# Kernel tuning notes

Hardware: AMD Instinct MI355X
Metric: run time of the kernel (lower is better)

Reference implementation:

```python
import jax, jax.numpy as jnp
import numpy as np

V, E, H = 50257, 256, 256   # vocab/output_size, embed_size, hidden_size
T, B = 4096, 64             # encoder time steps, batch


def setup_inputs() -> dict:
    key = jax.random.key(0)
    ks = jax.random.split(key, 12)
    s = 0.05
    return {
        "input_ids": jax.random.randint(ks[0], (B,), 0, V),
        "hidden": jax.random.normal(ks[1], (1, B, H), dtype=jnp.float32) * s,
        "encoder_outputs": jax.random.normal(ks[2], (T, B, 2 * H), dtype=jnp.float32) * s,
        # learned parameters (PyTorch Linear convention: W @ x.T, W shape (out, in))
        "emb": jax.random.normal(ks[3], (V, E), dtype=jnp.float32) * s,
        "W_attn": jax.random.normal(ks[4], (H, 3 * H), dtype=jnp.float32) * s,
        "b_attn": jnp.zeros((H,), jnp.float32),
        "v": jax.random.normal(ks[5], (H,), dtype=jnp.float32) * s,
        "W_comb": jax.random.normal(ks[6], (H, 2 * H + E), dtype=jnp.float32) * s,
        "b_comb": jnp.zeros((H,), jnp.float32),
        "W_ih": jax.random.normal(ks[7], (3 * H, H), dtype=jnp.float32) * s,
        "W_hh": jax.random.normal(ks[8], (3 * H, H), dtype=jnp.float32) * s,
        "b_ih": jnp.zeros((3 * H,), jnp.float32),
        "b_hh": jnp.zeros((3 * H,), jnp.float32),
        "W_out": jax.random.normal(ks[9], (V, 3 * H), dtype=jnp.float32) * s,
        "b_out": jnp.zeros((V,), jnp.float32),
    }


def reference(input_ids, hidden, encoder_outputs, emb, W_attn, b_attn, v,
              W_comb, b_comb, W_ih, W_hh, b_ih, b_hh, W_out, b_out):
    Tn, Bn, _ = encoder_outputs.shape
    Hn = hidden.shape[-1]
    embedded = emb[input_ids]                 # (B, E)
    h0 = hidden[0]                            # (B, H)

    # additive (Bahdanau) attention: energies over time axis
    h_rep = jnp.broadcast_to(h0[None], (Tn, Bn, Hn))            # (T, B, H)
    cat = jnp.concatenate([h_rep, encoder_outputs], axis=2)     # (T, B, 3H)
    energies = jnp.tanh(cat @ W_attn.T + b_attn)                # (T, B, H)
    scores = jnp.einsum('tbh,h->tb', energies, v)               # (T, B)
    attn = jax.nn.softmax(scores, axis=0)                       # softmax over time
    context = jnp.einsum('tb,tbd->bd', attn, encoder_outputs)   # (B, 2H)

    # combine context with embedded input
    comb = jnp.concatenate([context, embedded], axis=1) @ W_comb.T + b_comb  # (B, H)

    # single GRU step (PyTorch gate order: r, z, n)
    gx = comb @ W_ih.T + b_ih                 # (B, 3H)
    gh = h0 @ W_hh.T + b_hh                   # (B, 3H)
    xr, xz, xn = jnp.split(gx, 3, axis=1)
    hr, hz, hn = jnp.split(gh, 3, axis=1)
    r = jax.nn.sigmoid(xr + hr)
    z = jax.nn.sigmoid(xz + hz)
    n = jnp.tanh(xn + r * hn)
    h_new = (1.0 - z) * n + z * h0            # (B, H)

    logits = jnp.concatenate([h_new, context], axis=1) @ W_out.T + b_out  # (B, V)
    logp = jax.nn.log_softmax(logits, axis=1)
    return logp, h_new[None]                  # hidden_i shape (1, B, H)
```

## Files before the change

### kernel.cpp

```cpp
#include <hip/hip_runtime.h>
#include <hip/hip_bf16.h>
#include <cstdint>
#include <cstddef>

#define Tn 4096
#define Bn 64
#define Hn 256
#define En 256
#define Vn 50257
#define D2H 512
#define K3H 768

typedef __attribute__((ext_vector_type(8))) short short8;
typedef __attribute__((ext_vector_type(4))) float f32x4;

__device__ __forceinline__ short bfs(float f)
{
    __hip_bfloat16 h = __float2bfloat16(f);
    return *reinterpret_cast<short*>(&h);
}

__device__ __forceinline__ short8 pack8(const float4 x0, const float4 x1)
{
    short8 r;
    r[0] = bfs(x0.x); r[1] = bfs(x0.y); r[2] = bfs(x0.z); r[3] = bfs(x0.w);
    r[4] = bfs(x1.x); r[5] = bfs(x1.y); r[6] = bfs(x1.z); r[7] = bfs(x1.w);
    return r;
}

__device__ __forceinline__ uint2 pack4(const float4 v)
{
    uint2 r;
    r.x = (unsigned)(unsigned short)bfs(v.x) | ((unsigned)(unsigned short)bfs(v.y) << 16);
    r.y = (unsigned)(unsigned short)bfs(v.z) | ((unsigned)(unsigned short)bfs(v.w) << 16);
    return r;
}

__device__ __forceinline__ float bf2f(unsigned short u)
{
    return __uint_as_float(((unsigned)u) << 16);
}


__global__ __launch_bounds__(256) void k1_embed_base(
    const int* __restrict__ ids, const float* __restrict__ hidden,
    const float* __restrict__ emb, const float* __restrict__ W_attn,
    const float* __restrict__ b_attn,
    float* __restrict__ baseB, float* __restrict__ emb_g)
{
    const int b = blockIdx.x, h = threadIdx.x;
    __shared__ float h0[Hn];
    h0[h] = hidden[b * Hn + h];
    __syncthreads();
    float acc = b_attn[h];
    const float* wrow = W_attn + (size_t)h * K3H;
#pragma unroll 8
    for (int k = 0; k < Hn; ++k) acc += wrow[k] * h0[k];
    baseB[b * Hn + h] = acc;
    const int id = ids[b];
    emb_g[b * En + h] = emb[(size_t)id * En + h];
}

__global__ __launch_bounds__(64) void k1b_w2frag(
    const float* __restrict__ W_attn, unsigned short* __restrict__ w2frag)
{
    const int blk = blockIdx.x;
    const int nt = blk >> 4, kb = blk & 15;
    const int l = threadIdx.x, lr = l & 15, lg = l >> 4;
    const int h = nt * 16 + lr;
    const float* src = W_attn + (size_t)h * K3H + Hn + kb * 32 + lg * 8;
    float4 x0 = *reinterpret_cast<const float4*>(src);
    float4 x1 = *reinterpret_cast<const float4*>(src + 4);
    reinterpret_cast<short8*>(w2frag)[(size_t)blk * 64 + l] = pack8(x0, x1);
}

__global__ __launch_bounds__(256, 2) void k2f_attn(
    const float* __restrict__ enc, const unsigned short* __restrict__ w2frag,
    const float* __restrict__ vvec, const float* __restrict__ baseB,
    float* __restrict__ part, float2* __restrict__ meta)
{
    const int tid = threadIdx.x;
    const int bx  = blockIdx.x;
    const int b   = bx & 63;
    const int cid = bx >> 6;
    const int l = tid & 63;
    const int w = tid >> 6;
    const int lr = l & 15, lg = l >> 4;

    __shared__ unsigned short abf[64][520];
    __shared__ float red[64][5];
    __shared__ float wts[64];

    f32x4 acc[4][4];
    const f32x4 zero = {0.f, 0.f, 0.f, 0.f};
#pragma unroll
    for (int mi = 0; mi < 4; ++mi)
#pragma unroll
        for (int ni = 0; ni < 4; ++ni) acc[mi][ni] = zero;

    const short8* wf = reinterpret_cast<const short8*>(w2frag);

    const float* gbase = enc + ((size_t)(cid * 64 + w * 16 + lg) * Bn + b) * D2H
                       + lr * 4;

#define LOADREG(dst, c) do {                                                  \
    _Pragma("unroll")                                                         \
    for (int u = 0; u < 4; ++u)                                               \
        dst[u] = *reinterpret_cast<const float4*>(                            \
            gbase + (size_t)u * 131072 + (c) * 64);                           \
    } while (0)

#define WRITEC(src, c) do {                                                   \
    _Pragma("unroll")                                                         \
    for (int u = 0; u < 4; ++u)                                               \
        *reinterpret_cast<uint2*>(&abf[w * 16 + u * 4 + lg][(c) * 64 + lr * 4])\
            = pack4(src[u]);                                                  \
    } while (0)

#define COMPUTE_KB(kb, bfr) do {                                              \
    _Pragma("unroll")                                                         \
    for (int mi = 0; mi < 4; ++mi) {                                          \
        short8 a = *reinterpret_cast<const short8*>(                          \
            &abf[mi * 16 + lr][(kb) * 32 + lg * 8]);                          \
        _Pragma("unroll")                                                     \
        for (int ni = 0; ni < 4; ++ni)                                        \
            acc[mi][ni] = __builtin_amdgcn_mfma_f32_16x16x32_bf16(            \
                a, bfr[ni], acc[mi][ni], 0, 0, 0);                            \
    } } while (0)

    float4 st0[4], st1[4], st2[4];
    LOADREG(st0, 0);
    LOADREG(st1, 1);
    LOADREG(st2, 2);
    WRITEC(st0, 0);
    asm volatile("s_waitcnt lgkmcnt(0)" ::: "memory");
    __builtin_amdgcn_s_barrier();
    __builtin_amdgcn_sched_barrier(0);

#pragma unroll
    for (int kc = 0; kc < 8; ++kc) {
        short8 bfr0[4], bfr1[4];
#pragma unroll
        for (int ni = 0; ni < 4; ++ni)
            bfr0[ni] = wf[(size_t)(((w * 4 + ni) * 16) + 2 * kc) * 64 + l];
#pragma unroll
        for (int ni = 0; ni < 4; ++ni)
            bfr1[ni] = wf[(size_t)(((w * 4 + ni) * 16) + 2 * kc + 1) * 64 + l];
        __builtin_amdgcn_sched_barrier(0);
        if (kc < 5) {
            if ((kc % 3) == 0)      LOADREG(st0, kc + 3);
            else if ((kc % 3) == 1) LOADREG(st1, kc + 3);
            else                    LOADREG(st2, kc + 3);
        }
        COMPUTE_KB(2 * kc,     bfr0);
        COMPUTE_KB(2 * kc + 1, bfr1);
        if (kc < 7) {
            const int wb = (kc + 1) % 3;
            if (wb == 0)      WRITEC(st0, kc + 1);
            else if (wb == 1) WRITEC(st1, kc + 1);
            else              WRITEC(st2, kc + 1);
        }
        asm volatile("s_waitcnt lgkmcnt(0)" ::: "memory");
        __builtin_amdgcn_s_barrier();
        __builtin_amdgcn_sched_barrier(0);
    }
#undef LOADREG
#undef WRITEC
#undef COMPUTE_KB

    float psum[4][4];
#pragma unroll
    for (int mi = 0; mi < 4; ++mi)
#pragma unroll
        for (int r = 0; r < 4; ++r) psum[mi][r] = 0.f;
#pragma unroll
    for (int ni = 0; ni < 4; ++ni) {
        const int h = w * 64 + ni * 16 + lr;
        const float vh = vvec[h];
        const float bt = baseB[b * Hn + h];
#pragma unroll
        for (int mi = 0; mi < 4; ++mi)
#pragma unroll
            for (int r = 0; r < 4; ++r)
                psum[mi][r] += vh * tanhf(acc[mi][ni][r] + bt);
    }
#pragma unroll
    for (int d = 1; d < 16; d <<= 1)
#pragma unroll
        for (int mi = 0; mi < 4; ++mi)
#pragma unroll
            for (int r = 0; r < 4; ++r)
                psum[mi][r] += __shfl_xor(psum[mi][r], d, 64);
    if (lr == 0) {
#pragma unroll
        for (int mi = 0; mi < 4; ++mi)
#pragma unroll
            for (int r = 0; r < 4; ++r)
                red[mi * 16 + lg * 4 + r][w] = psum[mi][r];
    }
    __syncthreads();

    if (tid < 64) {
        float s = red[tid][0] + red[tid][1] + red[tid][2] + red[tid][3];
        float m = s;
#pragma unroll
        for (int d = 1; d < 64; d <<= 1) m = fmaxf(m, __shfl_xor(m, d, 64));
        const float e = expf(s - m);
        float lsum = e;
#pragma unroll
        for (int d = 1; d < 64; d <<= 1) lsum += __shfl_xor(lsum, d, 64);
        wts[tid] = e;
        if (tid == 0) meta[bx] = make_float2(m, lsum);
    }
    __syncthreads();

    const int d0 = tid * 2;
    float c0 = 0.f, c1 = 0.f;
#pragma unroll 4
    for (int t = 0; t < 64; ++t) {
        const float wt = wts[t];
        const unsigned u = *reinterpret_cast<const unsigned*>(&abf[t][d0]);
        c0 += wt * bf2f((unsigned short)(u & 0xffffu));
        c1 += wt * bf2f((unsigned short)(u >> 16));
    }
    float* pp = part + (size_t)bx * 512 + d0;
    pp[0] = c0; pp[1] = c1;
}

__global__ __launch_bounds__(256) void k56_ctx_gru(
    const float* __restrict__ part, const float2* __restrict__ meta,
    const float* __restrict__ hidden, const float* __restrict__ emb_g,
    const float* __restrict__ W_comb, const float* __restrict__ b_comb,
    const float* __restrict__ W_ih, const float* __restrict__ W_hh,
    const float* __restrict__ b_ih, const float* __restrict__ b_hh,
    float* __restrict__ y, float* __restrict__ out_hidden)
{
    const int b = blockIdx.x, tid = threadIdx.x;
    __shared__ float sc[64];
    __shared__ float in_[K3H];
    __shared__ float h0[Hn];
    __shared__ float comb[Hn];
    __shared__ float gx[K3H], gh[K3H];
    if (tid < 64) {
        const float2 ml = meta[(size_t)tid * 64 + b];
        float M = ml.x;
#pragma unroll
        for (int d = 1; d < 64; d <<= 1) M = fmaxf(M, __shfl_xor(M, d, 64));
        const float e = expf(ml.x - M);
        float L = e * ml.y;
#pragma unroll
        for (int d = 1; d < 64; d <<= 1) L += __shfl_xor(L, d, 64);
        sc[tid] = e / L;
    }
    in_[512 + tid] = emb_g[b * En + tid];
    h0[tid] = hidden[b * Hn + tid];
    __syncthreads();
    {
        const int d0 = tid * 2;
        float c0 = 0.f, c1 = 0.f;
#pragma unroll 4
        for (int c = 0; c < 64; ++c) {
            const float s = sc[c];
            const float2 p = *reinterpret_cast<const float2*>(
                part + ((size_t)c * 64 + b) * 512 + d0);
            c0 += s * p.x; c1 += s * p.y;
        }
        in_[d0] = c0; in_[d0 + 1] = c1;
        y[(size_t)b * K3H + Hn + d0]     = c0;
        y[(size_t)b * K3H + Hn + d0 + 1] = c1;
    }
    __syncthreads();
    {
        float c = b_comb[tid];
        const float* wr = W_comb + (size_t)tid * K3H;
#pragma unroll 8
        for (int k = 0; k < K3H; ++k) c += wr[k] * in_[k];
        comb[tid] = c;
    }
    __syncthreads();
#pragma unroll
    for (int p = 0; p < 3; ++p) {
        const int g = p * 256 + tid;
        float a = b_ih[g], bh = b_hh[g];
        const float* wi = W_ih + (size_t)g * Hn;
        const float* wh = W_hh + (size_t)g * Hn;
#pragma unroll 8
        for (int k = 0; k < Hn; ++k) { a += wi[k] * comb[k]; bh += wh[k] * h0[k]; }
        gx[g] = a; gh[g] = bh;
    }
    __syncthreads();
    const float r = 1.f / (1.f + expf(-(gx[tid] + gh[tid])));
    const float z = 1.f / (1.f + expf(-(gx[256 + tid] + gh[256 + tid])));
    const float n = tanhf(gx[512 + tid] + r * gh[512 + tid]);
    const float hn = (1.f - z) * n + z * h0[tid];
    y[(size_t)b * K3H + tid] = hn;
    out_hidden[b * Hn + tid] = hn;
}

__global__ __launch_bounds__(64) void k7y_pack(
    const float* __restrict__ y, unsigned short* __restrict__ yfrag)
{
    const int blk = blockIdx.x;
    const int ni = blk / 24, kb = blk % 24;
    const int l = threadIdx.x, lr = l & 15, lg = l >> 4;
    const int b = ni * 16 + lr;
    const float* src = y + (size_t)b * K3H + kb * 32 + lg * 8;
    float4 x0 = *reinterpret_cast<const float4*>(src);
    float4 x1 = *reinterpret_cast<const float4*>(src + 4);
    reinterpret_cast<short8*>(yfrag)[(size_t)blk * 64 + l] = pack8(x0, x1);
}

__global__ __launch_bounds__(256) void k7_logits(
    const float* __restrict__ W_out, const float* __restrict__ b_out,
    const unsigned short* __restrict__ yfrag, float* __restrict__ out)
{
    const int tid = threadIdx.x;
    const int vbase = blockIdx.x * 64;
    const int l = tid & 63, w = tid >> 6;
    const int lr = l & 15, lg = l >> 4;

    const short8* yf = reinterpret_cast<const short8*>(yfrag);

    f32x4 acc[4];
    const f32x4 zero = {0.f, 0.f, 0.f, 0.f};
#pragma unroll
    for (int ni = 0; ni < 4; ++ni) acc[ni] = zero;

    int v = vbase + w * 16 + lr;
    if (v >= Vn) v = Vn - 1;
    const float* wrow = W_out + (size_t)v * K3H + lg * 8;

#pragma unroll 4
    for (int kb = 0; kb < 24; ++kb) {
        float4 x0 = *reinterpret_cast<const float4*>(wrow + kb * 32);
        float4 x1 = *reinterpret_cast<const float4*>(wrow + kb * 32 + 4);
        short8 a = pack8(x0, x1);
#pragma unroll
        for (int ni = 0; ni < 4; ++ni) {
            short8 bf = yf[(size_t)(ni * 24 + kb) * 64 + l];
            acc[ni] = __builtin_amdgcn_mfma_f32_16x16x32_bf16(
                a, bf, acc[ni], 0, 0, 0);
        }
    }

    __shared__ float lt[64][65];
#pragma unroll
    for (int ni = 0; ni < 4; ++ni)
#pragma unroll
        for (int r = 0; r < 4; ++r)
            lt[w * 16 + lg * 4 + r][ni * 16 + lr] = acc[ni][r];
    __syncthreads();

#pragma unroll
    for (int u = 0; u < 16; ++u) {
        const int idx = tid + u * 256;
        const int bb = idx >> 6, vv = idx & 63;
        const int vo = vbase + vv;
        if (vo < Vn)
            out[(size_t)bb * Vn + vo] = lt[vv][bb] + b_out[vo];
    }
}

#define VQ 12565

__global__ __launch_bounds__(1024) void k8a_partial(
    const float* __restrict__ out, float2* __restrict__ qmeta)
{
    const int b = blockIdx.x, q = blockIdx.y;
    const int lo = q * VQ, hi = (lo + VQ < Vn) ? lo + VQ : Vn;
    const float* row = out + (size_t)b * Vn;
    __shared__ float red[1024];
    float m = -1e30f;
    for (int i = lo + threadIdx.x; i < hi; i += 1024) m = fmaxf(m, row[i]);
    red[threadIdx.x] = m; __syncthreads();
    for (int s = 512; s > 0; s >>= 1) {
        if (threadIdx.x < s) red[threadIdx.x] = fmaxf(red[threadIdx.x], red[threadIdx.x + s]);
        __syncthreads();
    }
    m = red[0]; __syncthreads();
    float l = 0.f;
    for (int i = lo + threadIdx.x; i < hi; i += 1024) l += expf(row[i] - m);
    red[threadIdx.x] = l; __syncthreads();
    for (int s = 512; s > 0; s >>= 1) {
        if (threadIdx.x < s) red[threadIdx.x] += red[threadIdx.x + s];
        __syncthreads();
    }
    if (threadIdx.x == 0) qmeta[b * 4 + q] = make_float2(m, red[0]);
}

__global__ __launch_bounds__(1024) void k8b_apply(
    float* __restrict__ out, const float2* __restrict__ qmeta)
{
    const int b = blockIdx.x, q = blockIdx.y;
    const int lo = q * VQ, hi = (lo + VQ < Vn) ? lo + VQ : Vn;
    float2 q0 = qmeta[b * 4 + 0], q1 = qmeta[b * 4 + 1];
    float2 q2 = qmeta[b * 4 + 2], q3 = qmeta[b * 4 + 3];
    const float M = fmaxf(fmaxf(q0.x, q1.x), fmaxf(q2.x, q3.x));
    const float L = q0.y * expf(q0.x - M) + q1.y * expf(q1.x - M)
                  + q2.y * expf(q2.x - M) + q3.y * expf(q3.x - M);
    const float off = M + logf(L);
    float* row = out + (size_t)b * Vn;
    for (int i = lo + threadIdx.x; i < hi; i += 1024) row[i] -= off;
}

extern "C" void kernel_launch(void* const* d_in, const int* in_sizes, int n_in,
                              void* d_out, int out_size, void* d_ws, size_t ws_size,
                              hipStream_t stream)
{
    const int*   ids    = (const int*)d_in[0];
    const float* hidden = (const float*)d_in[1];
    const float* enc    = (const float*)d_in[2];
    const float* emb    = (const float*)d_in[3];
    const float* W_attn = (const float*)d_in[4];
    const float* b_attn = (const float*)d_in[5];
    const float* vvec   = (const float*)d_in[6];
    const float* W_comb = (const float*)d_in[7];
    const float* b_comb = (const float*)d_in[8];
    const float* W_ih   = (const float*)d_in[9];
    const float* W_hh   = (const float*)d_in[10];
    const float* b_ih   = (const float*)d_in[11];
    const float* b_hh   = (const float*)d_in[12];
    const float* W_out  = (const float*)d_in[13];
    const float* b_out  = (const float*)d_in[14];

    float* out = (float*)d_out;
    float* ws = (float*)d_ws;
    float*  baseB = ws;
    float*  emb_g = ws + 16384;
    float2* meta  = (float2*)(ws + 32768);
    float*  part  = ws + 40960;
    float*  y     = ws + 2138112;
    unsigned short* w2frag = (unsigned short*)(ws + 2187264);
    unsigned short* yfrag  = (unsigned short*)(ws + 2252800);
    float2* qmeta = (float2*)(ws + 2277376);

    hipLaunchKernelGGL(k1_embed_base, dim3(Bn), dim3(256), 0, stream,
                       ids, hidden, emb, W_attn, b_attn, baseB, emb_g);
    hipLaunchKernelGGL(k1b_w2frag, dim3(256), dim3(64), 0, stream,
                       W_attn, w2frag);
    hipLaunchKernelGGL(k2f_attn, dim3(4096), dim3(256), 0, stream,
                       enc, w2frag, vvec, baseB, part, meta);
    hipLaunchKernelGGL(k56_ctx_gru, dim3(Bn), dim3(256), 0, stream,
                       part, meta, hidden, emb_g, W_comb, b_comb,
                       W_ih, W_hh, b_ih, b_hh, y, out + (size_t)Bn * Vn);
    hipLaunchKernelGGL(k7y_pack, dim3(96), dim3(64), 0, stream, y, yfrag);
    hipLaunchKernelGGL(k7_logits, dim3((Vn + 63) / 64), dim3(256), 0, stream,
                       W_out, b_out, yfrag, out);
    hipLaunchKernelGGL(k8a_partial, dim3(Bn, 4), dim3(1024), 0, stream,
                       out, qmeta);
    hipLaunchKernelGGL(k8b_apply, dim3(Bn, 4), dim3(1024), 0, stream,
                       out, qmeta);
}
```

Before: 341.9 us.

## Replace pipelined load/compute loop with bulk LDS load then unpipelined MFMA loop

The software-pipelined attention GEMM, which interleaved global encoder loads, LDS writes and MFMA compute across eight chunks with per-chunk barriers, is replaced by a two-phase structure. All encoder chunks are first loaded and written to LDS as bf16 (two chunks in flight per iteration), followed by a single barrier and then a plain 16-step MFMA loop. This drops the per-chunk barriers and the register pressure of three staging buffers, which may help occupancy. In exchange it gives up overlapping memory loads with MFMA work inside a block and relies on the two resident blocks per CU to hide latency.

```diff
diff --git a/kernel.cpp b/kernel.cpp
--- a/kernel.cpp
+++ b/kernel.cpp
@@ -91,15 +91,6 @@
     __shared__ float red[64][5];
     __shared__ float wts[64];
 
-    f32x4 acc[4][4];
-    const f32x4 zero = {0.f, 0.f, 0.f, 0.f};
-#pragma unroll
-    for (int mi = 0; mi < 4; ++mi)
-#pragma unroll
-        for (int ni = 0; ni < 4; ++ni) acc[mi][ni] = zero;
-
-    const short8* wf = reinterpret_cast<const short8*>(w2frag);
-
     const float* gbase = enc + ((size_t)(cid * 64 + w * 16 + lg) * Bn + b) * D2H
                        + lr * 4;
 
@@ -117,56 +108,45 @@
             = pack4(src[u]);                                                  \
     } while (0)
 
-#define COMPUTE_KB(kb, bfr) do {                                              \
-    _Pragma("unroll")                                                         \
-    for (int mi = 0; mi < 4; ++mi) {                                          \
-        short8 a = *reinterpret_cast<const short8*>(                          \
-            &abf[mi * 16 + lr][(kb) * 32 + lg * 8]);                          \
-        _Pragma("unroll")                                                     \
-        for (int ni = 0; ni < 4; ++ni)                                        \
-            acc[mi][ni] = __builtin_amdgcn_mfma_f32_16x16x32_bf16(            \
-                a, bfr[ni], acc[mi][ni], 0, 0, 0);                            \
-    } } while (0)
-
-    float4 st0[4], st1[4], st2[4];
-    LOADREG(st0, 0);
-    LOADREG(st1, 1);
-    LOADREG(st2, 2);
-    WRITEC(st0, 0);
-    asm volatile("s_waitcnt lgkmcnt(0)" ::: "memory");
-    __builtin_amdgcn_s_barrier();
-    __builtin_amdgcn_sched_barrier(0);
-
-#pragma unroll
-    for (int kc = 0; kc < 8; ++kc) {
-        short8 bfr0[4], bfr1[4];
+    {
+        float4 st0[4], st1[4];
+#pragma unroll 1
+        for (int kc = 0; kc < 8; kc += 2) {
+            LOADREG(st0, kc);
+            LOADREG(st1, kc + 1);
+            WRITEC(st0, kc);
+            WRITEC(st1, kc + 1);
+        }
+    }
+    __syncthreads();
+
+    f32x4 acc[4][4];
+    const f32x4 zero = {0.f, 0.f, 0.f, 0.f};
+#pragma unroll
+    for (int mi = 0; mi < 4; ++mi)
+#pragma unroll
+        for (int ni = 0; ni < 4; ++ni) acc[mi][ni] = zero;
+
+    const short8* wf = reinterpret_cast<const short8*>(w2frag);
+
+#pragma unroll
+    for (int kb = 0; kb < 16; ++kb) {
+        short8 bfr[4];
 #pragma unroll
         for (int ni = 0; ni < 4; ++ni)
-            bfr0[ni] = wf[(size_t)(((w * 4 + ni) * 16) + 2 * kc) * 64 + l];
-#pragma unroll
-        for (int ni = 0; ni < 4; ++ni)
-            bfr1[ni] = wf[(size_t)(((w * 4 + ni) * 16) + 2 * kc + 1) * 64 + l];
-        __builtin_amdgcn_sched_barrier(0);
-        if (kc < 5) {
-            if ((kc % 3) == 0)      LOADREG(st0, kc + 3);
-            else if ((kc % 3) == 1) LOADREG(st1, kc + 3);
-            else                    LOADREG(st2, kc + 3);
+            bfr[ni] = wf[(size_t)(((w * 4 + ni) * 16) + kb) * 64 + l];
+#pragma unroll
+        for (int mi = 0; mi < 4; ++mi) {
+            short8 a = *reinterpret_cast<const short8*>(
+                &abf[mi * 16 + lr][kb * 32 + lg * 8]);
+#pragma unroll
+            for (int ni = 0; ni < 4; ++ni)
+                acc[mi][ni] = __builtin_amdgcn_mfma_f32_16x16x32_bf16(
+                    a, bfr[ni], acc[mi][ni], 0, 0, 0);
         }
-        COMPUTE_KB(2 * kc,     bfr0);
-        COMPUTE_KB(2 * kc + 1, bfr1);
-        if (kc < 7) {
-            const int wb = (kc + 1) % 3;
-            if (wb == 0)      WRITEC(st0, kc + 1);
-            else if (wb == 1) WRITEC(st1, kc + 1);
-            else              WRITEC(st2, kc + 1);
-        }
-        asm volatile("s_waitcnt lgkmcnt(0)" ::: "memory");
-        __builtin_amdgcn_s_barrier();
-        __builtin_amdgcn_sched_barrier(0);
     }
 #undef LOADREG
 #undef WRITEC
-#undef COMPUTE_KB
 
     float psum[4][4];
 #pragma unroll
```

Result: no change. 348.6 us (+2.0%).
